# Performance work log

Measured on AMD Instinct MI355X. Metric: run time of the kernel, lower is better.

The kernel has to match this reference:

```python
import jax, jax.numpy as jnp
import numpy as np
from jax import lax

NUM_TAGS = 256
BATCH = 64
SEQ_LEN = 1024


def setup_inputs() -> dict:
    key = jax.random.key(0)
    k1, k2, k3, k4, k5 = jax.random.split(key, 5)
    inputs = jax.random.normal(k1, (BATCH, SEQ_LEN, NUM_TAGS), dtype=jnp.float32)
    tags = jax.random.randint(k2, (BATCH, SEQ_LEN), 0, NUM_TAGS, dtype=jnp.int64)
    mask = jnp.ones((BATCH, SEQ_LEN), dtype=bool)
    transitions = jax.random.normal(k3, (NUM_TAGS, NUM_TAGS), dtype=jnp.float32)
    start_transitions = jax.random.normal(k4, (NUM_TAGS,), dtype=jnp.float32)
    stop_transitions = jax.random.normal(k5, (NUM_TAGS,), dtype=jnp.float32)
    return {
        "inputs": inputs,
        "tags": tags,
        "mask": mask,
        "transitions": transitions,
        "start_transitions": start_transitions,
        "stop_transitions": stop_transitions,
    }


def _log_partition(inputs, mask, transitions, start_transitions, stop_transitions):
    # inputs: (B, L, T); mask: (B, L) bool
    # alpha_0[b, j] = start[j] + emit[b, 0, j]
    alpha0 = start_transitions[None, :] + inputs[:, 0]  # (B, T)

    def step(alpha, xs):
        emit_t, mask_t = xs  # (B, T), (B,)
        # inner[b, i, j] = alpha[b, i] + transitions[i, j] + emit_t[b, j]
        inner = alpha[:, :, None] + transitions[None, :, :] + emit_t[:, None, :]
        new_alpha = jax.nn.logsumexp(inner, axis=1)  # (B, T)
        alpha = jnp.where(mask_t[:, None], new_alpha, alpha)
        return alpha, None

    emits = jnp.swapaxes(inputs[:, 1:], 0, 1)  # (L-1, B, T)
    masks = jnp.swapaxes(mask[:, 1:], 0, 1)    # (L-1, B)
    alpha, _ = lax.scan(step, alpha0, (emits, masks))
    return jax.nn.logsumexp(alpha + stop_transitions[None, :], axis=-1)  # (B,)


def _log_score(inputs, tags, mask, transitions, start_transitions, stop_transitions):
    dtype = inputs.dtype
    maskf = mask.astype(dtype)  # (B, L)
    # per-step emission score for the gold tag: (B, L)
    emit = jnp.take_along_axis(inputs, tags[:, :, None], axis=2)[:, :, 0]
    # transition scores between consecutive gold tags: (B, L-1)
    trans_sc = transitions[tags[:, :-1], tags[:, 1:]]
    score = start_transitions[tags[:, 0]]
    score = score + jnp.sum(trans_sc * maskf[:, 1:] + emit[:, :-1] * maskf[:, :-1], axis=1)
    score = score + (stop_transitions[tags[:, -1]] + emit[:, -1]) * maskf[:, -1]
    return score  # (B,)


def reference(inputs, tags, mask, transitions, start_transitions, stop_transitions):
    log_denominator = _log_partition(inputs, mask, transitions, start_transitions, stop_transitions)
    log_numerator = _log_score(inputs, tags, mask, transitions, start_transitions, stop_transitions)
    return log_numerator - log_denominator  # (B,) per-sequence log-likelihood
```

## Files before the change

kernel.cpp:

```cpp
#include <hip/hip_runtime.h>
#include <math.h>

#define NUM_TAGS 256
#define BATCH 64
#define SEQ 1024
#define NT 512
#define NCHUNK 64
#define CH 16
#define BURN 8
#define PSTR 264
#define ESTR 260
#define RD 4

typedef _Float16 f16x8 __attribute__((ext_vector_type(8)));
typedef float f32x4 __attribute__((ext_vector_type(4)));

__device__ __forceinline__ void barrier_lgkm() {
    asm volatile("" ::: "memory");
    __builtin_amdgcn_s_waitcnt(0xC07F);
    __builtin_amdgcn_s_barrier();
    asm volatile("" ::: "memory");
}

__device__ __forceinline__ void gload_lds(const float* g, float* l) {
    __builtin_amdgcn_global_load_lds(
        (const __attribute__((address_space(1))) void*)g,
        (__attribute__((address_space(3))) void*)l, 16, 0, 0);
}

__global__ __attribute__((amdgpu_flat_work_group_size(NT, NT),
                          amdgpu_waves_per_eu(2, 2)))
void crf_mfma(const float* __restrict__ x, const int* __restrict__ tags,
              const float* __restrict__ T, const float* __restrict__ start,
              const float* __restrict__ stop, float* __restrict__ ws,
              float* __restrict__ out) {

    __shared__ __align__(16) float Ering[RD][16][ESTR];
    __shared__ __align__(16) _Float16 Pl[16 * PSTR];
    __shared__ float scale_s[16];
    __shared__ int win_s;

    const int bb   = blockIdx.x;
    const int c    = bb >> 2;
    const int g    = bb & 3;
    const int c0   = g << 4;
    const int tid  = threadIdx.x;
    const int lane = tid & 63;
    const int w    = tid >> 6;
    const int quad = lane >> 4;
    const int l15  = lane & 15;
    const int colw = (w << 5) + l15;

    float* p3  = ws;
    float* Cc  = ws + BATCH * NUM_TAGS;
    float* scp = Cc + BATCH * NCHUNK;
    int*   cnt = (int*)(scp + BATCH * 3);
    const int CNT_INIT = (int)0xAAAAAAAA;

    const int s0   = (c == 0) ? 1 : (1 - BURN);
    const int sEnd = (c == NCHUNK - 1) ? (CH - 1) : CH;

    const float* xw0 = x + (size_t)(c0 + w)     * SEQ * NUM_TAGS + (lane << 2);
    const float* xw1 = x + (size_t)(c0 + w + 8) * SEQ * NUM_TAGS + (lane << 2);

    auto issue = [&](int s_for, int slot) {
        int tt = c * CH + s_for; if (tt > SEQ - 1) tt = SEQ - 1;
        gload_lds(xw0 + (size_t)tt * NUM_TAGS, &Ering[slot][w][0]);
        gload_lds(xw1 + (size_t)tt * NUM_TAGS, &Ering[slot][w + 8][0]);
    };

#pragma unroll
    for (int d = 0; d < RD; ++d) issue(s0 + d, d);

    f16x8 Bf[8][2];
#pragma unroll
    for (int f = 0; f < 8; ++f)
#pragma unroll
        for (int jt = 0; jt < 2; ++jt)
#pragma unroll
            for (int i = 0; i < 8; ++i)
                Bf[f][jt][i] = (_Float16)__expf(
                    T[(size_t)(32 * f + 8 * quad + i) * NUM_TAGS + colw + 16 * jt]);

    const float* xr[4];
#pragma unroll
    for (int r = 0; r < 4; ++r)
        xr[r] = x + (size_t)(c0 + quad * 4 + r) * SEQ * NUM_TAGS;

    float Creg[4];
    if (c == 0) {
        float s0v = start[0];
#pragma unroll
        for (int r = 0; r < 4; ++r) {
            float a00 = s0v + xr[r][0];
            Creg[r] = a00;
#pragma unroll
            for (int jt = 0; jt < 2; ++jt) {
                int col = colw + 16 * jt;
                float v = __expf(start[col] + xr[r][col] - a00);
                Pl[(quad * 4 + r) * PSTR + col] = (_Float16)v;
            }
        }
    } else {
#pragma unroll
        for (int r = 0; r < 4; ++r) {
            Creg[r] = 0.0f;
#pragma unroll
            for (int jt = 0; jt < 2; ++jt)
                Pl[(quad * 4 + r) * PSTR + colw + 16 * jt] = (_Float16)1.0f;
        }
    }
    asm volatile("s_waitcnt vmcnt(0)" ::: "memory");
    barrier_lgkm();

    f16x8 Af[8];
#pragma unroll
    for (int f = 0; f < 8; ++f)
        Af[f] = *(const f16x8*)&Pl[l15 * PSTR + 32 * f + 8 * quad];

    for (int s = s0; s <= sEnd; ++s) {
        const int slot = (s - s0) & (RD - 1);
        f32x4 acc0 = {0.f, 0.f, 0.f, 0.f}, acc1 = {0.f, 0.f, 0.f, 0.f};
#pragma unroll
        for (int f = 0; f < 8; ++f) {
            acc0 = __builtin_amdgcn_mfma_f32_16x16x32_f16(Af[f], Bf[f][0], acc0, 0, 0, 0);
            acc1 = __builtin_amdgcn_mfma_f32_16x16x32_f16(Af[f], Bf[f][1], acc1, 0, 0, 0);
        }
        float v[8];
#pragma unroll
        for (int i = 0; i < 8; ++i) {
            int jt = i >> 2, r = i & 3;
            float em = Ering[slot][quad * 4 + r][colw + 16 * jt];
            float a = (jt == 0) ? acc0[r] : acc1[r];
            v[i] = a * __expf(em);
        }
        if (w == 0 && l15 == 0) {
#pragma unroll
            for (int r = 0; r < 4; ++r) scale_s[quad * 4 + r] = v[r];
        }
        barrier_lgkm();
        float rr[4];
#pragma unroll
        for (int r = 0; r < 4; ++r) rr[r] = __frcp_rn(scale_s[quad * 4 + r]);
        if (w == 0 && l15 == 0) {
#pragma unroll
            for (int r = 0; r < 4; ++r) {
                Creg[r] += __logf(scale_s[quad * 4 + r]);
                if (s <= 0) Creg[r] = 0.0f;
            }
        }
#pragma unroll
        for (int i = 0; i < 8; ++i) {
            int jt = i >> 2, r = i & 3;
            Pl[(quad * 4 + r) * PSTR + colw + 16 * jt] = (_Float16)(v[i] * rr[r]);
        }
        issue(s + RD, slot);
        asm volatile("s_waitcnt vmcnt(6)" ::: "memory");
        barrier_lgkm();
#pragma unroll
        for (int f = 0; f < 8; ++f)
            Af[f] = *(const f16x8*)&Pl[l15 * PSTR + 32 * f + 8 * quad];
    }

    if (w == 0 && l15 == 0) {
#pragma unroll
        for (int r = 0; r < 4; ++r)
            Cc[(size_t)(c0 + quad * 4 + r) * NCHUNK + c] = Creg[r];
    }
    if (c == NCHUNK - 1) {
#pragma unroll
        for (int q2 = 0; q2 < 8; ++q2) {
            int lin = tid * 8 + q2;
            int row = lin >> 8, col = lin & 255;
            p3[(size_t)(c0 + row) * NUM_TAGS + col] = (float)Pl[row * PSTR + col];
        }
    }

    {
        const int rank = bb >> 2;
        float term = 0.0f;
        const int lc = rank >> 1;
        const int chain = c0 + lc;
        if (rank < 32) {
            int t = ((rank & 1) << 9) + tid;
            if (t < SEQ - 1) {
                const int* tg = tags + (size_t)chain * SEQ;
                int a = tg[t], b2 = tg[t + 1];
                term = x[(size_t)chain * SEQ * NUM_TAGS + (size_t)t * NUM_TAGS + a]
                     + T[(size_t)a * NUM_TAGS + b2];
            }
        }
#pragma unroll
        for (int off = 32; off > 0; off >>= 1) term += __shfl_xor(term, off, 64);
        if (lane == 0) scale_s[w] = term;
        barrier_lgkm();
        if (rank < 32 && tid == 0)
            scp[chain * 3 + (rank & 1)] = scale_s[0] + scale_s[1] + scale_s[2] +
                                          scale_s[3] + scale_s[4] + scale_s[5] +
                                          scale_s[6] + scale_s[7];
        if (rank == 0 && tid < 16) {
            int ch2 = c0 + tid;
            const int* tg = tags + (size_t)ch2 * SEQ;
            int tl = tg[SEQ - 1];
            scp[ch2 * 3 + 2] = start[tg[0]] + stop[tl] +
                x[(size_t)ch2 * SEQ * NUM_TAGS + (size_t)(SEQ - 1) * NUM_TAGS + tl];
        }
    }

    __threadfence();
    if (tid == 0) win_s = (atomicAdd(&cnt[g], 1) == CNT_INIT + NCHUNK - 1);
    __syncthreads();
    if (win_s) {
        __threadfence();
        int lc = tid >> 5, sub = tid & 31;
        int chain = c0 + lc;
        float S = 0.0f;
        for (int j = sub; j < NUM_TAGS; j += 32)
            S += p3[(size_t)chain * NUM_TAGS + j] * __expf(stop[j]);
#pragma unroll
        for (int off = 16; off > 0; off >>= 1) S += __shfl_xor(S, off, 32);
        if (sub == 0) {
            float Cs = 0.0f;
            for (int cc2 = 0; cc2 < NCHUNK; ++cc2)
                Cs += Cc[(size_t)chain * NCHUNK + cc2];
            float score = scp[chain * 3] + scp[chain * 3 + 1] + scp[chain * 3 + 2];
            out[chain] = score - (Cs + __logf(S));
        }
    }
}

extern "C" void kernel_launch(void* const* d_in, const int* in_sizes, int n_in,
                              void* d_out, int out_size, void* d_ws, size_t ws_size,
                              hipStream_t stream) {
    const float* x     = (const float*)d_in[0];
    const int*   tags  = (const int*)d_in[1];
    const float* T     = (const float*)d_in[3];
    const float* start = (const float*)d_in[4];
    const float* stop  = (const float*)d_in[5];
    float* out = (float*)d_out;
    float* ws  = (float*)d_ws;

    crf_mfma<<<4 * NCHUNK, NT, 0, stream>>>(x, tags, T, start, stop, ws, out);
}
```

Baseline: 174.1 us.

## Halve block size, double-buffer P, and drop per-step scale-exchange barrier

Each block now runs 4 waves instead of 8, and every wave computes 64 columns with 4 MFMA accumulators, so each wave does more work between barriers. Per-step normalisation now uses the previous step's P[*,0] value read from a double-buffered LDS tile, scaled by a constant. This removes the extra barrier that existed only to broadcast the scale factors, leaving one barrier per recurrence step. The cost is more registers per wave (occupancy is set to one wave per EU), fewer threads for the loads and the score reduction, and a risk of fp16 overflow or underflow from the lagged scaling.

```diff
diff --git a/kernel.cpp b/kernel.cpp
--- a/kernel.cpp
+++ b/kernel.cpp
@@ -4,13 +4,15 @@
 #define NUM_TAGS 256
 #define BATCH 64
 #define SEQ 1024
-#define NT 512
+#define NT 256
 #define NCHUNK 64
 #define CH 16
 #define BURN 8
 #define PSTR 264
 #define ESTR 260
 #define RD 4
+#define LNK 7.6246189861593985f
+#define RK  4.8828125e-4f
 
 typedef _Float16 f16x8 __attribute__((ext_vector_type(8)));
 typedef float f32x4 __attribute__((ext_vector_type(4)));
@@ -29,15 +31,15 @@
 }
 
 __global__ __attribute__((amdgpu_flat_work_group_size(NT, NT),
-                          amdgpu_waves_per_eu(2, 2)))
+                          amdgpu_waves_per_eu(1, 1)))
 void crf_mfma(const float* __restrict__ x, const int* __restrict__ tags,
               const float* __restrict__ T, const float* __restrict__ start,
               const float* __restrict__ stop, float* __restrict__ ws,
               float* __restrict__ out) {
 
     __shared__ __align__(16) float Ering[RD][16][ESTR];
-    __shared__ __align__(16) _Float16 Pl[16 * PSTR];
-    __shared__ float scale_s[16];
+    __shared__ __align__(16) _Float16 Pl[2][16 * PSTR];
+    __shared__ float red_s[4];
     __shared__ int win_s;
 
     const int bb   = blockIdx.x;
@@ -49,56 +51,57 @@
     const int w    = tid >> 6;
     const int quad = lane >> 4;
     const int l15  = lane & 15;
-    const int colw = (w << 5) + l15;
+    const int colw = (w << 6) + l15;
 
     float* p3  = ws;
     float* Cc  = ws + BATCH * NUM_TAGS;
     float* scp = Cc + BATCH * NCHUNK;
-    int*   cnt = (int*)(scp + BATCH * 3);
+    int*   cnt = (int*)(scp + BATCH * 5);
     const int CNT_INIT = (int)0xAAAAAAAA;
 
     const int s0   = (c == 0) ? 1 : (1 - BURN);
     const int sEnd = (c == NCHUNK - 1) ? (CH - 1) : CH;
 
-    const float* xw0 = x + (size_t)(c0 + w)     * SEQ * NUM_TAGS + (lane << 2);
-    const float* xw1 = x + (size_t)(c0 + w + 8) * SEQ * NUM_TAGS + (lane << 2);
+    const float* xg[4];
+#pragma unroll
+    for (int j = 0; j < 4; ++j)
+        xg[j] = x + (size_t)(c0 + 4 * w + j) * SEQ * NUM_TAGS + (lane << 2);
 
     auto issue = [&](int s_for, int slot) {
-        int tt = c * CH + s_for; if (tt > SEQ - 1) tt = SEQ - 1;
-        gload_lds(xw0 + (size_t)tt * NUM_TAGS, &Ering[slot][w][0]);
-        gload_lds(xw1 + (size_t)tt * NUM_TAGS, &Ering[slot][w + 8][0]);
+        int tt = c * CH + s_for;
+        if (tt < 0) tt = 0;
+        if (tt > SEQ - 1) tt = SEQ - 1;
+#pragma unroll
+        for (int j = 0; j < 4; ++j)
+            gload_lds(xg[j] + (size_t)tt * NUM_TAGS, &Ering[slot][4 * w + j][0]);
     };
 
 #pragma unroll
-    for (int d = 0; d < RD; ++d) issue(s0 + d, d);
-
-    f16x8 Bf[8][2];
+    for (int d = 0; d < RD - 1; ++d) issue(s0 + d, d);
+
+    f16x8 Bf[8][4];
 #pragma unroll
     for (int f = 0; f < 8; ++f)
 #pragma unroll
-        for (int jt = 0; jt < 2; ++jt)
+        for (int jt = 0; jt < 4; ++jt)
 #pragma unroll
             for (int i = 0; i < 8; ++i)
                 Bf[f][jt][i] = (_Float16)__expf(
                     T[(size_t)(32 * f + 8 * quad + i) * NUM_TAGS + colw + 16 * jt]);
 
-    const float* xr[4];
-#pragma unroll
-    for (int r = 0; r < 4; ++r)
-        xr[r] = x + (size_t)(c0 + quad * 4 + r) * SEQ * NUM_TAGS;
-
     float Creg[4];
     if (c == 0) {
         float s0v = start[0];
 #pragma unroll
         for (int r = 0; r < 4; ++r) {
-            float a00 = s0v + xr[r][0];
+            const float* xr = x + (size_t)(c0 + quad * 4 + r) * SEQ * NUM_TAGS;
+            float a00 = s0v + xr[0];
             Creg[r] = a00;
 #pragma unroll
-            for (int jt = 0; jt < 2; ++jt) {
+            for (int jt = 0; jt < 4; ++jt) {
                 int col = colw + 16 * jt;
-                float v = __expf(start[col] + xr[r][col] - a00);
-                Pl[(quad * 4 + r) * PSTR + col] = (_Float16)v;
+                float v = __expf(start[col] + xr[col] - a00);
+                Pl[1][(quad * 4 + r) * PSTR + col] = (_Float16)v;
             }
         }
     } else {
@@ -106,103 +109,116 @@
         for (int r = 0; r < 4; ++r) {
             Creg[r] = 0.0f;
 #pragma unroll
-            for (int jt = 0; jt < 2; ++jt)
-                Pl[(quad * 4 + r) * PSTR + colw + 16 * jt] = (_Float16)1.0f;
+            for (int jt = 0; jt < 4; ++jt)
+                Pl[1][(quad * 4 + r) * PSTR + colw + 16 * jt] = (_Float16)1.0f;
         }
     }
     asm volatile("s_waitcnt vmcnt(0)" ::: "memory");
     barrier_lgkm();
 
     f16x8 Af[8];
+    float p0v[4];
 #pragma unroll
     for (int f = 0; f < 8; ++f)
-        Af[f] = *(const f16x8*)&Pl[l15 * PSTR + 32 * f + 8 * quad];
+        Af[f] = *(const f16x8*)&Pl[1][l15 * PSTR + 32 * f + 8 * quad];
+#pragma unroll
+    for (int r = 0; r < 4; ++r)
+        p0v[r] = (float)Pl[1][(quad * 4 + r) * PSTR + 0];
 
     for (int s = s0; s <= sEnd; ++s) {
         const int slot = (s - s0) & (RD - 1);
-        f32x4 acc0 = {0.f, 0.f, 0.f, 0.f}, acc1 = {0.f, 0.f, 0.f, 0.f};
-#pragma unroll
-        for (int f = 0; f < 8; ++f) {
-            acc0 = __builtin_amdgcn_mfma_f32_16x16x32_f16(Af[f], Bf[f][0], acc0, 0, 0, 0);
-            acc1 = __builtin_amdgcn_mfma_f32_16x16x32_f16(Af[f], Bf[f][1], acc1, 0, 0, 0);
-        }
-        float v[8];
-#pragma unroll
-        for (int i = 0; i < 8; ++i) {
-            int jt = i >> 2, r = i & 3;
-            float em = Ering[slot][quad * 4 + r][colw + 16 * jt];
-            float a = (jt == 0) ? acc0[r] : acc1[r];
-            v[i] = a * __expf(em);
-        }
-        if (w == 0 && l15 == 0) {
-#pragma unroll
-            for (int r = 0; r < 4; ++r) scale_s[quad * 4 + r] = v[r];
-        }
+        const int pwb  = (s - s0) & 1;
+
+        float rr[4];
+#pragma unroll
+        for (int r = 0; r < 4; ++r) rr[r] = __frcp_rn(p0v[r]) * RK;
+
+        f32x4 acc[4];
+#pragma unroll
+        for (int jt = 0; jt < 4; ++jt) acc[jt] = (f32x4){0.f, 0.f, 0.f, 0.f};
+#pragma unroll
+        for (int f = 0; f < 8; ++f)
+#pragma unroll
+            for (int jt = 0; jt < 4; ++jt)
+                acc[jt] = __builtin_amdgcn_mfma_f32_16x16x32_f16(
+                    Af[f], Bf[f][jt], acc[jt], 0, 0, 0);
+
+        float vjr[4][4];
+#pragma unroll
+        for (int r = 0; r < 4; ++r) {
+            const float* er = &Ering[slot][quad * 4 + r][colw];
+            float e0 = er[0], e1 = er[16], e2 = er[32], e3 = er[48];
+            vjr[0][r] = acc[0][r] * __expf(e0);
+            vjr[1][r] = acc[1][r] * __expf(e1);
+            vjr[2][r] = acc[2][r] * __expf(e2);
+            vjr[3][r] = acc[3][r] * __expf(e3);
+        }
+
+#pragma unroll
+        for (int jt = 0; jt < 4; ++jt)
+#pragma unroll
+            for (int r = 0; r < 4; ++r)
+                Pl[pwb][(quad * 4 + r) * PSTR + colw + 16 * jt] =
+                    (_Float16)(vjr[jt][r] * rr[r]);
+
+        if (w == 0 && l15 == 0 && s >= 1) {
+#pragma unroll
+            for (int r = 0; r < 4; ++r)
+                Creg[r] += LNK + ((s == 1) ? 0.0f : __logf(p0v[r]));
+        }
+
+        issue(s + RD - 1, (s + RD - 1 - s0) & (RD - 1));
+        asm volatile("s_waitcnt vmcnt(8)" ::: "memory");
         barrier_lgkm();
-        float rr[4];
-#pragma unroll
-        for (int r = 0; r < 4; ++r) rr[r] = __frcp_rn(scale_s[quad * 4 + r]);
-        if (w == 0 && l15 == 0) {
-#pragma unroll
-            for (int r = 0; r < 4; ++r) {
-                Creg[r] += __logf(scale_s[quad * 4 + r]);
-                if (s <= 0) Creg[r] = 0.0f;
-            }
-        }
-#pragma unroll
-        for (int i = 0; i < 8; ++i) {
-            int jt = i >> 2, r = i & 3;
-            Pl[(quad * 4 + r) * PSTR + colw + 16 * jt] = (_Float16)(v[i] * rr[r]);
-        }
-        issue(s + RD, slot);
-        asm volatile("s_waitcnt vmcnt(6)" ::: "memory");
+#pragma unroll
+        for (int f = 0; f < 8; ++f)
+            Af[f] = *(const f16x8*)&Pl[pwb][l15 * PSTR + 32 * f + 8 * quad];
+#pragma unroll
+        for (int r = 0; r < 4; ++r)
+            p0v[r] = (float)Pl[pwb][(quad * 4 + r) * PSTR + 0];
+    }
+
+    if (w == 0 && l15 == 0) {
+#pragma unroll
+        for (int r = 0; r < 4; ++r) {
+            float cr = Creg[r];
+            if (c != NCHUNK - 1) cr += __logf(p0v[r]);
+            Cc[(size_t)(c0 + quad * 4 + r) * NCHUNK + c] = cr;
+        }
+    }
+    if (c == NCHUNK - 1) {
+        const int fb = (sEnd - s0) & 1;
+#pragma unroll
+        for (int q2 = 0; q2 < 16; ++q2) {
+            int lin = tid * 16 + q2;
+            int row = lin >> 8, col = lin & 255;
+            p3[(size_t)(c0 + row) * NUM_TAGS + col] = (float)Pl[fb][row * PSTR + col];
+        }
+    }
+
+    {
+        const int rank  = c;
+        const int chain = c0 + (rank >> 2);
+        const int q4    = rank & 3;
+        const int t     = (q4 << 8) + tid;
+        float term = 0.0f;
+        if (t < SEQ - 1) {
+            const int* tg = tags + (size_t)chain * SEQ;
+            int a = tg[t], b2 = tg[t + 1];
+            term = x[(size_t)chain * SEQ * NUM_TAGS + (size_t)t * NUM_TAGS + a]
+                 + T[(size_t)a * NUM_TAGS + b2];
+        }
+#pragma unroll
+        for (int off = 32; off > 0; off >>= 1) term += __shfl_xor(term, off, 64);
+        if (lane == 0) red_s[w] = term;
         barrier_lgkm();
-#pragma unroll
-        for (int f = 0; f < 8; ++f)
-            Af[f] = *(const f16x8*)&Pl[l15 * PSTR + 32 * f + 8 * quad];
-    }
-
-    if (w == 0 && l15 == 0) {
-#pragma unroll
-        for (int r = 0; r < 4; ++r)
-            Cc[(size_t)(c0 + quad * 4 + r) * NCHUNK + c] = Creg[r];
-    }
-    if (c == NCHUNK - 1) {
-#pragma unroll
-        for (int q2 = 0; q2 < 8; ++q2) {
-            int lin = tid * 8 + q2;
-            int row = lin >> 8, col = lin & 255;
-            p3[(size_t)(c0 + row) * NUM_TAGS + col] = (float)Pl[row * PSTR + col];
-        }
-    }
-
-    {
-        const int rank = bb >> 2;
-        float term = 0.0f;
-        const int lc = rank >> 1;
-        const int chain = c0 + lc;
-        if (rank < 32) {
-            int t = ((rank & 1) << 9) + tid;
-            if (t < SEQ - 1) {
-                const int* tg = tags + (size_t)chain * SEQ;
-                int a = tg[t], b2 = tg[t + 1];
-                term = x[(size_t)chain * SEQ * NUM_TAGS + (size_t)t * NUM_TAGS + a]
-                     + T[(size_t)a * NUM_TAGS + b2];
-            }
-        }
-#pragma unroll
-        for (int off = 32; off > 0; off >>= 1) term += __shfl_xor(term, off, 64);
-        if (lane == 0) scale_s[w] = term;
-        barrier_lgkm();
-        if (rank < 32 && tid == 0)
-            scp[chain * 3 + (rank & 1)] = scale_s[0] + scale_s[1] + scale_s[2] +
-                                          scale_s[3] + scale_s[4] + scale_s[5] +
-                                          scale_s[6] + scale_s[7];
+        if (tid == 0)
+            scp[chain * 5 + q4] = red_s[0] + red_s[1] + red_s[2] + red_s[3];
         if (rank == 0 && tid < 16) {
             int ch2 = c0 + tid;
             const int* tg = tags + (size_t)ch2 * SEQ;
             int tl = tg[SEQ - 1];
-            scp[ch2 * 3 + 2] = start[tg[0]] + stop[tl] +
+            scp[ch2 * 5 + 4] = start[tg[0]] + stop[tl] +
                 x[(size_t)ch2 * SEQ * NUM_TAGS + (size_t)(SEQ - 1) * NUM_TAGS + tl];
         }
     }
@@ -212,18 +228,22 @@
     __syncthreads();
     if (win_s) {
         __threadfence();
-        int lc = tid >> 5, sub = tid & 31;
+        int lc = tid >> 4, sub = tid & 15;
         int chain = c0 + lc;
         float S = 0.0f;
-        for (int j = sub; j < NUM_TAGS; j += 32)
+        for (int j = sub; j < NUM_TAGS; j += 16)
             S += p3[(size_t)chain * NUM_TAGS + j] * __expf(stop[j]);
-#pragma unroll
-        for (int off = 16; off > 0; off >>= 1) S += __shfl_xor(S, off, 32);
+        float Cs = 0.0f;
+        for (int cc2 = sub; cc2 < NCHUNK; cc2 += 16)
+            Cs += Cc[(size_t)chain * NCHUNK + cc2];
+#pragma unroll
+        for (int off = 8; off > 0; off >>= 1) {
+            S  += __shfl_xor(S, off, 16);
+            Cs += __shfl_xor(Cs, off, 16);
+        }
         if (sub == 0) {
-            float Cs = 0.0f;
-            for (int cc2 = 0; cc2 < NCHUNK; ++cc2)
-                Cs += Cc[(size_t)chain * NCHUNK + cc2];
-            float score = scp[chain * 3] + scp[chain * 3 + 1] + scp[chain * 3 + 2];
+            float score = scp[chain * 5] + scp[chain * 5 + 1] + scp[chain * 5 + 2]
+                        + scp[chain * 5 + 3] + scp[chain * 5 + 4];
             out[chain] = score - (Cs + __logf(S));
         }
     }
```

Result: faster. 160.5 us (-7.8%).
